# Kernel tuning notes

Measured on AMD Instinct MI355X. Metric: run time of the kernel, lower is better.

## Reference

```python
import jax, jax.numpy as jnp
import numpy as np

# Config constants (from init_kwargs)
B, T, D = 4, 2048, 2048      # batch, seq, d_model
E, R, F = 8, 8, 1024         # n_experts, gate_proj_rank, d_ff per expert
GATE_THRESHOLD = 0.0
GATE_TEMPERATURE = 1.0
W_INIT = 0.02                # standard small init scale


def setup_inputs() -> dict:
    key = jax.random.key(0)
    ks = jax.random.split(key, 6)
    hidden_states = jax.random.normal(ks[0], (B, T, D), jnp.float32)
    W_A = jax.random.normal(ks[1], (E, R, D), jnp.float32) * W_INIT      # low-rank gate proj per expert
    gate_scale = jnp.ones((E,), jnp.float32)
    # bias centered near typical score magnitude so the threshold mask is partially active
    gate_bias = 2.5 + 0.1 * jax.random.uniform(ks[2], (E,), jnp.float32)
    w_gate = jax.random.normal(ks[3], (E, F, D), jnp.float32) * W_INIT
    w_up = jax.random.normal(ks[4], (E, F, D), jnp.float32) * W_INIT
    w_down = jax.random.normal(ks[5], (E, D, F), jnp.float32) * W_INIT
    return {"hidden_states": hidden_states, "W_A": W_A, "gate_scale": gate_scale,
            "gate_bias": gate_bias, "w_gate": w_gate, "w_up": w_up, "w_down": w_down}


def reference(hidden_states, W_A, gate_scale, gate_bias, w_gate, w_up, w_down):
    orig_shape = hidden_states.shape
    x = hidden_states.reshape(-1, orig_shape[-1])                 # [N, D]
    threshold = GATE_THRESHOLD / GATE_TEMPERATURE

    # Shared low-rank gate projection for all experts (F.linear with concatenated W_A)
    gate_hidden = jnp.einsum('nd,erd->ner', x, W_A)               # [N, E, R]
    # _gate_norm: L2 norm over rank dim, divided by temperature -> [N, E]
    scores = jnp.sqrt(jnp.sum(gate_hidden * gate_hidden, axis=-1)) / GATE_TEMPERATURE
    # per-expert scale / bias
    scores = scores * gate_scale[None, :] - gate_bias[None, :]    # [N, E]
    mask = scores >= threshold                                    # [N, E] bool

    # Masked SwiGLU FFN per expert, vectorized over E (same math as the expert loop)
    h = jax.nn.silu(jnp.einsum('nd,efd->nef', x, w_gate)) * jnp.einsum('nd,efd->nef', x, w_up)  # [N, E, F]
    gate_w = jnp.where(mask, jax.nn.sigmoid(scores), 0.0)         # [N, E] masked gating weight
    out = jnp.einsum('nef,edf,ne->nd', h, w_down, gate_w)         # accumulate expert outputs
    out = out.reshape(orig_shape)

    # Scattered gate scores: -inf where expert inactive (stack over experts at dim=-1)
    score_full = jnp.where(mask, scores, -jnp.inf).reshape(orig_shape[:-1] + (E,))  # [B, T, E]
    return out, score_full
```

## Files before the change

### kernel.cpp

```cpp
#include <hip/hip_runtime.h>
#include <hip/hip_bf16.h>
#include <math.h>

#define NTOK   8192
#define DMODEL 2048
#define NEXP   8
#define RGATE  8
#define DFF    1024

#define NEG_SENTINEL (-3.0e38f)

using f32x4  = __attribute__((ext_vector_type(4))) float;
using short8 = __attribute__((ext_vector_type(8))) short;

static __device__ __forceinline__ short f2bf(float f) {
  union { float f; unsigned u; } v; v.f = f;
  unsigned r = v.u + 0x7fffu + ((v.u >> 16) & 1u);
  return (short)(r >> 16);
}
static __device__ __forceinline__ float bf2f(short s) {
  union { unsigned u; float f; } v; v.u = ((unsigned)(unsigned short)s) << 16;
  return v.f;
}
static __device__ __forceinline__ short8 cvt8(const float4 a, const float4 b) {
  short8 o;
  o[0] = f2bf(a.x); o[1] = f2bf(a.y); o[2] = f2bf(a.z); o[3] = f2bf(a.w);
  o[4] = f2bf(b.x); o[5] = f2bf(b.y); o[6] = f2bf(b.z); o[7] = f2bf(b.w);
  return o;
}

#define GLOAD_LDS(gp, lp)                                                  \
  __builtin_amdgcn_global_load_lds(                                        \
      (const __attribute__((address_space(1))) void*)(gp),                 \
      (__attribute__((address_space(3))) void*)(lp), 16, 0, 0)

__global__ __launch_bounds__(256) void prep_zero(
    float4* __restrict__ out4, int4* __restrict__ ic4, int nIc4, int zero_out) {
  const int stride = gridDim.x * blockDim.x;
  const float4 z4 = make_float4(0.f, 0.f, 0.f, 0.f);
  for (int i = blockIdx.x * blockDim.x + threadIdx.x;
       i < NTOK * DMODEL / 4; i += stride) {
    if (zero_out) out4[i] = z4;
    if (i < nIc4) ic4[i] = make_int4(0, 0, 0, 0);
    if (!zero_out && i >= nIc4) break;
  }
}

__global__ __launch_bounds__(256) void cvt_kernel(
    const float* __restrict__ in, short* __restrict__ out, int n8) {
  const int stride = gridDim.x * blockDim.x;
  for (int i = blockIdx.x * blockDim.x + threadIdx.x; i < n8; i += stride) {
    const float4 a = ((const float4*)in)[(size_t)i * 2];
    const float4 b = ((const float4*)in)[(size_t)i * 2 + 1];
    ((short8*)out)[i] = cvt8(a, b);
  }
}

__global__ __launch_bounds__(256) void pack_gu(
    const float* __restrict__ wg, const float* __restrict__ wu,
    short* __restrict__ wgu) {
  const int stride = gridDim.x * blockDim.x;
  const int total = NEXP * 2048 * (DMODEL / 8);
  for (int i = blockIdx.x * blockDim.x + threadIdx.x; i < total; i += stride) {
    const int c = i & 255;
    const int r = (i >> 8) & 2047;
    const int e = i >> 19;
    const int sel = (r >> 4) & 1;
    const int f = ((r >> 5) << 4) + (r & 15);
    const float* src = (sel ? wu : wg) + ((size_t)(e * DFF + f)) * DMODEL + c * 8;
    const float4 a = *(const float4*)src;
    const float4 b = *(const float4*)(src + 4);
    ((short8*)wgu)[i] = cvt8(a, b);
  }
}

__global__ __launch_bounds__(256) void gate_v3(
    const float* __restrict__ x, const float* __restrict__ W_A,
    const float* __restrict__ gscale, const float* __restrict__ gbias,
    float* __restrict__ gw, float* __restrict__ score_out,
    int* __restrict__ idx, int* __restrict__ pos, int* __restrict__ cnt) {
  __shared__ float ghs[32][65];
  const int tok0 = blockIdx.x * 32;
  const int t = threadIdx.x;
  const int ks = t & 3;
  const int posn = t >> 2;
  const int tg = posn & 7;
  const int rg = posn >> 3;
  const float* xp = x + (size_t)(tok0 + tg * 4) * DMODEL;
  const float* wp = W_A + (size_t)(rg * 8) * DMODEL;

  float acc[4][8];
#pragma unroll
  for (int i = 0; i < 4; ++i)
#pragma unroll
    for (int r = 0; r < 8; ++r) acc[i][r] = 0.f;

  float4 xa_[4], wa_[8], xb_[4], wb_[8];
  auto loadj = [&](int j, float4* xv, float4* wv) {
    const int k = ks * 4 + j * 16;
#pragma unroll
    for (int i = 0; i < 4; ++i) xv[i] = *(const float4*)(xp + (size_t)i * DMODEL + k);
#pragma unroll
    for (int r = 0; r < 8; ++r) wv[r] = *(const float4*)(wp + (size_t)r * DMODEL + k);
  };
  auto fmaj = [&](const float4* xv, const float4* wv) {
#pragma unroll
    for (int i = 0; i < 4; ++i)
#pragma unroll
      for (int r = 0; r < 8; ++r) {
        acc[i][r] = fmaf(xv[i].x, wv[r].x, acc[i][r]);
        acc[i][r] = fmaf(xv[i].y, wv[r].y, acc[i][r]);
        acc[i][r] = fmaf(xv[i].z, wv[r].z, acc[i][r]);
        acc[i][r] = fmaf(xv[i].w, wv[r].w, acc[i][r]);
      }
  };

  loadj(0, xa_, wa_);
#pragma unroll 1
  for (int j = 0; j < 128; j += 2) {
    loadj(j + 1, xb_, wb_);
    fmaj(xa_, wa_);
    if (j + 2 < 128) loadj(j + 2, xa_, wa_);
    fmaj(xb_, wb_);
  }

#pragma unroll
  for (int i = 0; i < 4; ++i)
#pragma unroll
    for (int r = 0; r < 8; ++r) {
      float v = acc[i][r];
      v += __shfl_xor(v, 1);
      v += __shfl_xor(v, 2);
      acc[i][r] = v;
    }
  if (ks == 0) {
#pragma unroll
    for (int i = 0; i < 4; ++i)
#pragma unroll
      for (int r = 0; r < 8; ++r) ghs[tg * 4 + i][rg * 8 + r] = acc[i][r];
  }
  __syncthreads();

  {
    const int tk = t >> 3, e = t & 7;
    const int n = tok0 + tk;
    float ss = 0.f;
#pragma unroll
    for (int r = 0; r < RGATE; ++r) { const float v = ghs[tk][e * 8 + r]; ss += v * v; }
    const float score = sqrtf(ss) * gscale[e] - gbias[e];
    const bool m = (score >= 0.0f);
    const float sig = 1.0f / (1.0f + expf(-score));
    gw[(size_t)n * NEXP + e] = m ? sig : 0.0f;
    score_out[(size_t)n * NEXP + e] = m ? score : NEG_SENTINEL;
    int slot = -1;
    if (m) {
      slot = atomicAdd(&cnt[e], 1);
      idx[(size_t)e * NTOK + slot] = n;
    }
    pos[(size_t)e * NTOK + n] = slot;
  }
}

#define FFN1_STAGE(AS, BS, k0)                                                 \
  _Pragma("unroll") for (int i_ = 0; i_ < 4; ++i_) {                           \
    const int row_ = wid * 32 + i_ * 8;                                        \
    GLOAD_LDS(xb + (size_t)tokA[i_] * DMODEL + (k0) + lk,                      \
              (char*)(AS) + row_ * 128);                                       \
    GLOAD_LDS(Bb + (size_t)(row_ + lr) * DMODEL + (k0) + lk,                   \
              (char*)(BS) + row_ * 128);                                       \
  }

#define FFN1_COMPUTE(AS, BS)                                                   \
  _Pragma("unroll") for (int ks_ = 0; ks_ < 2; ++ks_) {                        \
    const int cswz_ = ((ks_ * 4 + (lane >> 4)) ^ (lane & 7)) << 4;             \
    short8 af_[8], bf_[4];                                                     \
    _Pragma("unroll") for (int q_ = 0; q_ < 8; ++q_)                           \
      af_[q_] = *(const short8*)((const char*)(AS) +                           \
                (arow + q_ * 16 + (lane & 15)) * 128 + cswz_);                 \
    _Pragma("unroll") for (int q_ = 0; q_ < 4; ++q_)                           \
      bf_[q_] = *(const short8*)((const char*)(BS) +                           \
                (brow + q_ * 16 + (lane & 15)) * 128 + cswz_);                 \
    _Pragma("unroll") for (int nf_ = 0; nf_ < 8; ++nf_)                        \
      _Pragma("unroll") for (int ff_ = 0; ff_ < 4; ++ff_)                      \
        acc[nf_][ff_] = __builtin_amdgcn_mfma_f32_16x16x32_bf16(               \
            af_[nf_], bf_[ff_], acc[nf_][ff_], 0, 0, 0);                       \
  }

__global__ __launch_bounds__(512, 2) void ffn1_gemm256(
    const short* __restrict__ xb, const short* __restrict__ wgu,
    const int* __restrict__ idx, const int* __restrict__ cnt,
    const float* __restrict__ gw, short* __restrict__ Hb, int e_arg) {
  const int e = (e_arg < 0) ? (int)blockIdx.z : e_arg;
  short* __restrict__ Hbe = Hb + ((e_arg < 0) ? (size_t)e * NTOK * DFF : (size_t)0);
  const int cnte = cnt[e];
  const int n0 = blockIdx.y * 256;
  if (n0 >= cnte) return;

  __shared__ __align__(16) short As0[256 * 64];
  __shared__ __align__(16) short Bs0[256 * 64];
  __shared__ __align__(16) short As1[256 * 64];
  __shared__ __align__(16) short Bs1[256 * 64];

  const int c0 = blockIdx.x * 256;
  const int t = threadIdx.x, lane = t & 63, wid = t >> 6;
  const int arow = (wid >> 2) * 128;
  const int brow = (wid & 3) * 64;
  const int* idxe = idx + (size_t)e * NTOK;
  const short* Bb = wgu + (size_t)e * 2048 * DMODEL + (size_t)c0 * DMODEL;
  const int lr = lane >> 3;
  const int lk = ((lane & 7) ^ lr) * 8;

  int tokA[4];
#pragma unroll
  for (int i = 0; i < 4; ++i) tokA[i] = idxe[n0 + wid * 32 + i * 8 + lr];

  f32x4 acc[8][4];
#pragma unroll
  for (int i = 0; i < 8; ++i)
#pragma unroll
    for (int j = 0; j < 4; ++j) acc[i][j] = (f32x4){0.f, 0.f, 0.f, 0.f};

  FFN1_STAGE(As0, Bs0, 0);
  __syncthreads();
#pragma unroll 1
  for (int kt = 0; kt < 32; kt += 2) {
    FFN1_STAGE(As1, Bs1, (kt + 1) * 64);
    FFN1_COMPUTE(As0, Bs0);
    __syncthreads();
    if (kt + 2 < 32) FFN1_STAGE(As0, Bs0, (kt + 2) * 64);
    FFN1_COMPUTE(As1, Bs1);
    __syncthreads();
  }

  const int fhalf = c0 >> 1;
#pragma unroll
  for (int nf = 0; nf < 8; ++nf) {
#pragma unroll
    for (int j = 0; j < 4; ++j) {
      const int n = n0 + arow + nf * 16 + (lane >> 4) * 4 + j;
      const bool valid = n < cnte;
      const int tok = valid ? idxe[n] : 0;
      const float gwv = gw[(size_t)tok * NEXP + e];
#pragma unroll
      for (int p = 0; p < 2; ++p) {
        const float gv = acc[nf][2 * p][j];
        const float uv = acc[nf][2 * p + 1][j];
        const float h = (gv / (1.f + expf(-gv))) * uv * gwv;
        const int f = fhalf + ((wid & 3) * 2 + p) * 16 + (lane & 15);
        Hbe[(size_t)n * DFF + f] = valid ? f2bf(h) : (short)0;
      }
    }
  }
}

#define FFN2_STAGE(AS, BS, k0)                                                 \
  _Pragma("unroll") for (int i_ = 0; i_ < 4; ++i_) {                           \
    const int row_ = wid * 32 + i_ * 8;                                        \
    GLOAD_LDS(Ab + (size_t)(row_ + lr) * DFF + (k0) + lk,                      \
              (char*)(AS) + row_ * 128);                                       \
    GLOAD_LDS(Bb + (size_t)(row_ + lr) * DFF + (k0) + lk,                      \
              (char*)(BS) + row_ * 128);                                       \
  }

#define FFN2_COMPUTE(AS, BS)                                                   \
  _Pragma("unroll") for (int ks_ = 0; ks_ < 2; ++ks_) {                        \
    const int cswz_ = ((ks_ * 4 + (lane >> 4)) ^ (lane & 7)) << 4;             \
    short8 af_[4], bf_[4];                                                     \
    _Pragma("unroll") for (int q_ = 0; q_ < 4; ++q_) {                         \
      af_[q_] = *(const short8*)((const char*)(AS) +                           \
                (wr * 64 + q_ * 16 + (lane & 15)) * 128 + cswz_);              \
      bf_[q_] = *(const short8*)((const char*)(BS) +                           \
                (wc * 64 + q_ * 16 + (lane & 15)) * 128 + cswz_);              \
    }                                                                          \
    _Pragma("unroll") for (int nf_ = 0; nf_ < 4; ++nf_)                        \
      _Pragma("unroll") for (int ff_ = 0; ff_ < 4; ++ff_)                      \
        acc[nf_][ff_] = __builtin_amdgcn_mfma_f32_16x16x32_bf16(               \
            af_[nf_], bf_[ff_], acc[nf_][ff_], 0, 0, 0);                       \
  }

__global__ __launch_bounds__(256, 2) void ffn2z_gemm(
    const short* __restrict__ Hb, const short* __restrict__ wdb,
    const int* __restrict__ cnt, short* __restrict__ Cp, int e0) {
  const int e = e0 + blockIdx.z;
  const int cnte = cnt[e];
  const int n0 = blockIdx.y * 128;
  if (n0 >= cnte) return;
  __shared__ __align__(16) short As0[128 * 64];
  __shared__ __align__(16) short Bs0[128 * 64];
  __shared__ __align__(16) short As1[128 * 64];
  __shared__ __align__(16) short Bs1[128 * 64];

  const int c0 = blockIdx.x * 128;
  const int t = threadIdx.x, lane = t & 63, wid = t >> 6;
  const int wr = wid >> 1, wc = wid & 1;
  const short* Ab = Hb + (size_t)e * NTOK * DFF + (size_t)n0 * DFF;
  const short* Bb = wdb + (size_t)e * DMODEL * DFF + (size_t)c0 * DFF;
  short* Cpe = Cp + (size_t)blockIdx.z * NTOK * DMODEL;
  const int lr = lane >> 3;
  const int lk = ((lane & 7) ^ lr) * 8;

  f32x4 acc[4][4];
#pragma unroll
  for (int i = 0; i < 4; ++i)
#pragma unroll
    for (int j = 0; j < 4; ++j) acc[i][j] = (f32x4){0.f, 0.f, 0.f, 0.f};

  FFN2_STAGE(As0, Bs0, 0);
  __syncthreads();
#pragma unroll 1
  for (int kt = 0; kt < 16; kt += 2) {
    FFN2_STAGE(As1, Bs1, (kt + 1) * 64);
    FFN2_COMPUTE(As0, Bs0);
    __syncthreads();
    if (kt + 2 < 16) FFN2_STAGE(As0, Bs0, (kt + 2) * 64);
    FFN2_COMPUTE(As1, Bs1);
    __syncthreads();
  }

#pragma unroll
  for (int nf = 0; nf < 4; ++nf) {
#pragma unroll
    for (int j = 0; j < 4; ++j) {
      const int n = n0 + wr * 64 + nf * 16 + (lane >> 4) * 4 + j;
      if (n < cnte) {
#pragma unroll
        for (int ff = 0; ff < 4; ++ff) {
          const int d = c0 + wc * 64 + ff * 16 + (lane & 15);
          Cpe[(size_t)n * DMODEL + d] = f2bf(acc[nf][ff][j]);
        }
      }
    }
  }
}

__global__ __launch_bounds__(256) void reduce_out_g(
    const short* __restrict__ Cp, const int* __restrict__ pos,
    float* __restrict__ out, int e0, int ge, int accum) {
  const int n = blockIdx.x;
  const int t = threadIdx.x;
  float* op = out + (size_t)n * DMODEL + t * 8;
  float acc[8];
  if (accum) {
    const float4 a = *(const float4*)op;
    const float4 b = *(const float4*)(op + 4);
    acc[0] = a.x; acc[1] = a.y; acc[2] = a.z; acc[3] = a.w;
    acc[4] = b.x; acc[5] = b.y; acc[6] = b.z; acc[7] = b.w;
  } else {
#pragma unroll
    for (int j = 0; j < 8; ++j) acc[j] = 0.f;
  }
  for (int el = 0; el < ge; ++el) {
    const int p = pos[(size_t)(e0 + el) * NTOK + n];
    if (p >= 0) {
      const short8 v = *(const short8*)(Cp + (size_t)el * NTOK * DMODEL +
                                        (size_t)p * DMODEL + t * 8);
#pragma unroll
      for (int j = 0; j < 8; ++j) acc[j] += bf2f(v[j]);
    }
  }
  *(float4*)op = make_float4(acc[0], acc[1], acc[2], acc[3]);
  *(float4*)(op + 4) = make_float4(acc[4], acc[5], acc[6], acc[7]);
}

__global__ __launch_bounds__(256, 2) void ffn2_gemm_db(
    const short* __restrict__ Hbe, const short* __restrict__ wdb,
    const int* __restrict__ idx, const int* __restrict__ cnt,
    float* __restrict__ out, float* __restrict__ dummy, int e) {
  const int cnte = cnt[e];
  const int n0 = blockIdx.y * 128;
  if (n0 >= cnte) return;
  __shared__ __align__(16) short As0[128 * 64];
  __shared__ __align__(16) short Bs0[128 * 64];
  __shared__ __align__(16) short As1[128 * 64];
  __shared__ __align__(16) short Bs1[128 * 64];

  const int c0 = blockIdx.x * 128;
  const int t = threadIdx.x, lane = t & 63, wid = t >> 6;
  const int wr = wid >> 1, wc = wid & 1;
  const int* idxe = idx + (size_t)e * NTOK;
  const short* Ab = Hbe + (size_t)n0 * DFF;
  const short* Bb = wdb + (size_t)e * DMODEL * DFF + (size_t)c0 * DFF;
  const int lr = lane >> 3;
  const int lk = ((lane & 7) ^ lr) * 8;

  f32x4 acc[4][4];
#pragma unroll
  for (int i = 0; i < 4; ++i)
#pragma unroll
    for (int j = 0; j < 4; ++j) acc[i][j] = (f32x4){0.f, 0.f, 0.f, 0.f};

  FFN2_STAGE(As0, Bs0, 0);
  __syncthreads();
#pragma unroll 1
  for (int kt = 0; kt < 16; kt += 2) {
    FFN2_STAGE(As1, Bs1, (kt + 1) * 64);
    FFN2_COMPUTE(As0, Bs0);
    __syncthreads();
    if (kt + 2 < 16) FFN2_STAGE(As0, Bs0, (kt + 2) * 64);
    FFN2_COMPUTE(As1, Bs1);
    __syncthreads();
  }

#pragma unroll
  for (int nf = 0; nf < 4; ++nf) {
#pragma unroll
    for (int j = 0; j < 4; ++j) {
      const int n = n0 + wr * 64 + nf * 16 + (lane >> 4) * 4 + j;
      const bool valid = n < cnte;
      const int tok = valid ? idxe[n] : 0;
      float* bp = valid ? (out + (size_t)tok * DMODEL) : dummy;
#pragma unroll
      for (int ff = 0; ff < 4; ++ff) {
        const int d = c0 + wc * 64 + ff * 16 + (lane & 15);
        bp[valid ? d : (d & 2047)] += acc[nf][ff][j];
      }
    }
  }
}

extern "C" void kernel_launch(void* const* d_in, const int* in_sizes, int n_in,
                              void* d_out, int out_size, void* d_ws, size_t ws_size,
                              hipStream_t stream) {
  const float* x      = (const float*)d_in[0];
  const float* W_A    = (const float*)d_in[1];
  const float* gscale = (const float*)d_in[2];
  const float* gbias  = (const float*)d_in[3];
  const float* wg     = (const float*)d_in[4];
  const float* wu     = (const float*)d_in[5];
  const float* wd     = (const float*)d_in[6];

  float* out       = (float*)d_out;
  float* score_out = out + (size_t)NTOK * DMODEL;

  const size_t CNT = (size_t)16777216;
  const size_t CP_SLICE = (size_t)NTOK * DMODEL * 2;
  size_t off = 0;
  float* gw    = (float*)((char*)d_ws + off); off += (size_t)NTOK * NEXP * 4;
  int*   idx   = (int*)((char*)d_ws + off);   off += (size_t)NEXP * NTOK * 4;
  int*   pos   = (int*)((char*)d_ws + off);   off += (size_t)NEXP * NTOK * 4;
  int*   cnt   = (int*)((char*)d_ws + off);   off += 16 * 4;
  float* dummy = (float*)((char*)d_ws + off); off += (size_t)DMODEL * 4;
  short* wdb   = (short*)((char*)d_ws + off); off += CNT * 2;
  const size_t hb_off = off;
  short* Hb    = (short*)((char*)d_ws + off); off += (size_t)NEXP * NTOK * DFF * 2;
  const size_t xb_off = off;
  short* xb    = (short*)((char*)d_ws + off); off += CNT * 2;
  short* wgu   = (short*)((char*)d_ws + off); off += CNT * 4;
  const size_t needA = off;
  short* Cp    = (short*)((char*)d_ws + xb_off);

  const bool tierA = (ws_size >= needA);
  int G = 0;
  if (tierA) {
    size_t avail = ws_size - xb_off;
    G = (int)(avail / CP_SLICE);
    if (G > NEXP) G = NEXP;
  }

  short* HbB  = Hb;
  short* xbB  = (short*)((char*)d_ws + hb_off + (size_t)NTOK * DFF * 2);
  short* wguB = xbB + CNT;

  const int nIc4 = (int)((2 * NEXP * NTOK + 16) / 4);
  const int zero_out = (tierA && G >= 1) ? 0 : 1;
  prep_zero<<<2048, 256, 0, stream>>>((float4*)out, (int4*)idx, nIc4, zero_out);

  short* xbT  = tierA ? xb : xbB;
  short* wguT = tierA ? wgu : wguB;
  cvt_kernel<<<2048, 256, 0, stream>>>(x,  xbT,  (int)(CNT / 8));
  cvt_kernel<<<2048, 256, 0, stream>>>(wd, wdb, (int)(CNT / 8));
  pack_gu<<<2048, 256, 0, stream>>>(wg, wu, wguT);
  gate_v3<<<NTOK / 32, 256, 0, stream>>>(x, W_A, gscale, gbias, gw,
                                         score_out, idx, pos, cnt);

  if (tierA && G >= 1) {
    ffn1_gemm256<<<dim3(2048 / 256, NTOK / 256, NEXP), 512, 0, stream>>>(
        xb, wgu, idx, cnt, gw, Hb, -1);
    const int np = (NEXP + G - 1) / G;
    int e0 = 0;
    for (int p = 0; p < np; ++p) {
      const int rem_p = np - p;
      const int ge = (NEXP - e0 + rem_p - 1) / rem_p;
      ffn2z_gemm<<<dim3(DMODEL / 128, NTOK / 128, ge), 256, 0, stream>>>(
          Hb, wdb, cnt, Cp, e0);
      reduce_out_g<<<NTOK, 256, 0, stream>>>(Cp, pos, out, e0, ge, p > 0);
      e0 += ge;
    }
  } else if (tierA) {
    ffn1_gemm256<<<dim3(2048 / 256, NTOK / 256, NEXP), 512, 0, stream>>>(
        xb, wgu, idx, cnt, gw, Hb, -1);
    for (int e = 0; e < NEXP; ++e)
      ffn2_gemm_db<<<dim3(DMODEL / 128, NTOK / 128), 256, 0, stream>>>(
          Hb + (size_t)e * NTOK * DFF, wdb, idx, cnt, out, dummy, e);
  } else {
    for (int e = 0; e < NEXP; ++e) {
      ffn1_gemm256<<<dim3(2048 / 256, NTOK / 256), 512, 0, stream>>>(
          xbB, wguB, idx, cnt, gw, HbB, e);
      ffn2_gemm_db<<<dim3(DMODEL / 128, NTOK / 128), 256, 0, stream>>>(
          HbB, wdb, idx, cnt, out, dummy, e);
    }
  }
}
```

Baseline: 876.9 us.

## Fuse prep kernels into one and restructure MFMA loops with setprio

Merges the zeroing, x/w_down conversion and gate/up packing kernels into a single prep_all launch. It also stops clearing the idx buffer, resetting only the expert counters and clamping out-of-range token indices in ffn1. Both GEMM compute macros now load fragments for both k-steps up front, issue MFMAs in sub-blocks, and raise wave priority around the MFMA bursts. This cuts launch count and prep memory traffic, but the changed fragment ordering may raise register pressure in the GEMMs.

```diff
diff --git a/kernel.cpp b/kernel.cpp
--- a/kernel.cpp
+++ b/kernel.cpp
@@ -34,43 +34,42 @@
       (const __attribute__((address_space(1))) void*)(gp),                 \
       (__attribute__((address_space(3))) void*)(lp), 16, 0, 0)
 
-__global__ __launch_bounds__(256) void prep_zero(
-    float4* __restrict__ out4, int4* __restrict__ ic4, int nIc4, int zero_out) {
+#define SEG_CVT  2097152
+#define SEG_PACK 4194304
+__global__ __launch_bounds__(256) void prep_all(
+    const float* __restrict__ x, const float* __restrict__ wd,
+    const float* __restrict__ wg, const float* __restrict__ wu,
+    short* __restrict__ xb, short* __restrict__ wdb, short* __restrict__ wgu,
+    int* __restrict__ cnt, float4* __restrict__ out4, int zero_out) {
+  if (blockIdx.x == 0 && threadIdx.x < 16) cnt[threadIdx.x] = 0;
   const int stride = gridDim.x * blockDim.x;
-  const float4 z4 = make_float4(0.f, 0.f, 0.f, 0.f);
-  for (int i = blockIdx.x * blockDim.x + threadIdx.x;
-       i < NTOK * DMODEL / 4; i += stride) {
-    if (zero_out) out4[i] = z4;
-    if (i < nIc4) ic4[i] = make_int4(0, 0, 0, 0);
-    if (!zero_out && i >= nIc4) break;
-  }
-}
-
-__global__ __launch_bounds__(256) void cvt_kernel(
-    const float* __restrict__ in, short* __restrict__ out, int n8) {
-  const int stride = gridDim.x * blockDim.x;
-  for (int i = blockIdx.x * blockDim.x + threadIdx.x; i < n8; i += stride) {
-    const float4 a = ((const float4*)in)[(size_t)i * 2];
-    const float4 b = ((const float4*)in)[(size_t)i * 2 + 1];
-    ((short8*)out)[i] = cvt8(a, b);
-  }
-}
-
-__global__ __launch_bounds__(256) void pack_gu(
-    const float* __restrict__ wg, const float* __restrict__ wu,
-    short* __restrict__ wgu) {
-  const int stride = gridDim.x * blockDim.x;
-  const int total = NEXP * 2048 * (DMODEL / 8);
+  const int total = SEG_CVT * 2 + SEG_PACK + (zero_out ? SEG_CVT : 0);
   for (int i = blockIdx.x * blockDim.x + threadIdx.x; i < total; i += stride) {
-    const int c = i & 255;
-    const int r = (i >> 8) & 2047;
-    const int e = i >> 19;
-    const int sel = (r >> 4) & 1;
-    const int f = ((r >> 5) << 4) + (r & 15);
-    const float* src = (sel ? wu : wg) + ((size_t)(e * DFF + f)) * DMODEL + c * 8;
-    const float4 a = *(const float4*)src;
-    const float4 b = *(const float4*)(src + 4);
-    ((short8*)wgu)[i] = cvt8(a, b);
+    if (i < SEG_CVT) {
+      const float4 a = ((const float4*)x)[(size_t)i * 2];
+      const float4 b = ((const float4*)x)[(size_t)i * 2 + 1];
+      ((short8*)xb)[i] = cvt8(a, b);
+    } else if (i < 2 * SEG_CVT) {
+      const int j = i - SEG_CVT;
+      const float4 a = ((const float4*)wd)[(size_t)j * 2];
+      const float4 b = ((const float4*)wd)[(size_t)j * 2 + 1];
+      ((short8*)wdb)[j] = cvt8(a, b);
+    } else if (i < 2 * SEG_CVT + SEG_PACK) {
+      const int j = i - 2 * SEG_CVT;
+      const int c = j & 255;
+      const int r = (j >> 8) & 2047;
+      const int e = j >> 19;
+      const int sel = (r >> 4) & 1;
+      const int f = ((r >> 5) << 4) + (r & 15);
+      const float* src = (sel ? wu : wg) + ((size_t)(e * DFF + f)) * DMODEL + c * 8;
+      const float4 a = *(const float4*)src;
+      const float4 b = *(const float4*)(src + 4);
+      ((short8*)wgu)[j] = cvt8(a, b);
+    } else {
+      const int j = i - (2 * SEG_CVT + SEG_PACK);
+      out4[(size_t)j * 2] = make_float4(0.f, 0.f, 0.f, 0.f);
+      out4[(size_t)j * 2 + 1] = make_float4(0.f, 0.f, 0.f, 0.f);
+    }
   }
 }
 
@@ -170,20 +169,31 @@
               (char*)(BS) + row_ * 128);                                       \
   }
 
+#define CSWZ(ks_) ((((ks_) * 4 + (lane >> 4)) ^ (lane & 7)) << 4)
+
 #define FFN1_COMPUTE(AS, BS)                                                   \
-  _Pragma("unroll") for (int ks_ = 0; ks_ < 2; ++ks_) {                        \
-    const int cswz_ = ((ks_ * 4 + (lane >> 4)) ^ (lane & 7)) << 4;             \
-    short8 af_[8], bf_[4];                                                     \
-    _Pragma("unroll") for (int q_ = 0; q_ < 8; ++q_)                           \
-      af_[q_] = *(const short8*)((const char*)(AS) +                           \
-                (arow + q_ * 16 + (lane & 15)) * 128 + cswz_);                 \
+  _Pragma("unroll") for (int ah_ = 0; ah_ < 2; ++ah_) {                        \
+    short8 af_[4][2];                                                          \
     _Pragma("unroll") for (int q_ = 0; q_ < 4; ++q_)                           \
-      bf_[q_] = *(const short8*)((const char*)(BS) +                           \
-                (brow + q_ * 16 + (lane & 15)) * 128 + cswz_);                 \
-    _Pragma("unroll") for (int nf_ = 0; nf_ < 8; ++nf_)                        \
-      _Pragma("unroll") for (int ff_ = 0; ff_ < 4; ++ff_)                      \
-        acc[nf_][ff_] = __builtin_amdgcn_mfma_f32_16x16x32_bf16(               \
-            af_[nf_], bf_[ff_], acc[nf_][ff_], 0, 0, 0);                       \
+      _Pragma("unroll") for (int ks_ = 0; ks_ < 2; ++ks_)                      \
+        af_[q_][ks_] = *(const short8*)((const char*)(AS) +                    \
+            (arow + (ah_ * 4 + q_) * 16 + (lane & 15)) * 128 + CSWZ(ks_));     \
+    _Pragma("unroll") for (int bh_ = 0; bh_ < 2; ++bh_) {                      \
+      short8 bf_[2][2];                                                        \
+      _Pragma("unroll") for (int q_ = 0; q_ < 2; ++q_)                         \
+        _Pragma("unroll") for (int ks_ = 0; ks_ < 2; ++ks_)                    \
+          bf_[q_][ks_] = *(const short8*)((const char*)(BS) +                  \
+              (brow + (bh_ * 2 + q_) * 16 + (lane & 15)) * 128 + CSWZ(ks_));   \
+      __builtin_amdgcn_s_setprio(1);                                           \
+      _Pragma("unroll") for (int ks_ = 0; ks_ < 2; ++ks_)                      \
+        _Pragma("unroll") for (int nf_ = 0; nf_ < 4; ++nf_)                    \
+          _Pragma("unroll") for (int ff_ = 0; ff_ < 2; ++ff_)                  \
+            acc[ah_ * 4 + nf_][bh_ * 2 + ff_] =                                \
+                __builtin_amdgcn_mfma_f32_16x16x32_bf16(                       \
+                    af_[nf_][ks_], bf_[ff_][ks_],                              \
+                    acc[ah_ * 4 + nf_][bh_ * 2 + ff_], 0, 0, 0);               \
+      __builtin_amdgcn_s_setprio(0);                                           \
+    }                                                                          \
   }
 
 __global__ __launch_bounds__(512, 2) void ffn1_gemm256(
@@ -212,7 +222,11 @@
 
   int tokA[4];
 #pragma unroll
-  for (int i = 0; i < 4; ++i) tokA[i] = idxe[n0 + wid * 32 + i * 8 + lr];
+  for (int i = 0; i < 4; ++i) {
+    int n = n0 + wid * 32 + i * 8 + lr;
+    if (n >= cnte) n = cnte - 1;
+    tokA[i] = idxe[n];
+  }
 
   f32x4 acc[8][4];
 #pragma unroll
@@ -263,19 +277,28 @@
   }
 
 #define FFN2_COMPUTE(AS, BS)                                                   \
-  _Pragma("unroll") for (int ks_ = 0; ks_ < 2; ++ks_) {                        \
-    const int cswz_ = ((ks_ * 4 + (lane >> 4)) ^ (lane & 7)) << 4;             \
-    short8 af_[4], bf_[4];                                                     \
-    _Pragma("unroll") for (int q_ = 0; q_ < 4; ++q_) {                         \
-      af_[q_] = *(const short8*)((const char*)(AS) +                           \
-                (wr * 64 + q_ * 16 + (lane & 15)) * 128 + cswz_);              \
-      bf_[q_] = *(const short8*)((const char*)(BS) +                           \
-                (wc * 64 + q_ * 16 + (lane & 15)) * 128 + cswz_);              \
+  {                                                                            \
+    short8 af_[4][2];                                                          \
+    _Pragma("unroll") for (int q_ = 0; q_ < 4; ++q_)                           \
+      _Pragma("unroll") for (int ks_ = 0; ks_ < 2; ++ks_)                      \
+        af_[q_][ks_] = *(const short8*)((const char*)(AS) +                    \
+            (wr * 64 + q_ * 16 + (lane & 15)) * 128 + CSWZ(ks_));              \
+    _Pragma("unroll") for (int bh_ = 0; bh_ < 2; ++bh_) {                      \
+      short8 bf_[2][2];                                                        \
+      _Pragma("unroll") for (int q_ = 0; q_ < 2; ++q_)                         \
+        _Pragma("unroll") for (int ks_ = 0; ks_ < 2; ++ks_)                    \
+          bf_[q_][ks_] = *(const short8*)((const char*)(BS) +                  \
+              (wc * 64 + (bh_ * 2 + q_) * 16 + (lane & 15)) * 128 + CSWZ(ks_));\
+      __builtin_amdgcn_s_setprio(1);                                           \
+      _Pragma("unroll") for (int ks_ = 0; ks_ < 2; ++ks_)                      \
+        _Pragma("unroll") for (int nf_ = 0; nf_ < 4; ++nf_)                    \
+          _Pragma("unroll") for (int ff_ = 0; ff_ < 2; ++ff_)                  \
+            acc[nf_][bh_ * 2 + ff_] =                                          \
+                __builtin_amdgcn_mfma_f32_16x16x32_bf16(                       \
+                    af_[nf_][ks_], bf_[ff_][ks_],                              \
+                    acc[nf_][bh_ * 2 + ff_], 0, 0, 0);                         \
+      __builtin_amdgcn_s_setprio(0);                                           \
     }                                                                          \
-    _Pragma("unroll") for (int nf_ = 0; nf_ < 4; ++nf_)                        \
-      _Pragma("unroll") for (int ff_ = 0; ff_ < 4; ++ff_)                      \
-        acc[nf_][ff_] = __builtin_amdgcn_mfma_f32_16x16x32_bf16(               \
-            af_[nf_], bf_[ff_], acc[nf_][ff_], 0, 0, 0);                       \
   }
 
 __global__ __launch_bounds__(256, 2) void ffn2z_gemm(
@@ -461,15 +484,12 @@
   short* xbB  = (short*)((char*)d_ws + hb_off + (size_t)NTOK * DFF * 2);
   short* wguB = xbB + CNT;
 
-  const int nIc4 = (int)((2 * NEXP * NTOK + 16) / 4);
   const int zero_out = (tierA && G >= 1) ? 0 : 1;
-  prep_zero<<<2048, 256, 0, stream>>>((float4*)out, (int4*)idx, nIc4, zero_out);
-
   short* xbT  = tierA ? xb : xbB;
   short* wguT = tierA ? wgu : wguB;
-  cvt_kernel<<<2048, 256, 0, stream>>>(x,  xbT,  (int)(CNT / 8));
-  cvt_kernel<<<2048, 256, 0, stream>>>(wd, wdb, (int)(CNT / 8));
-  pack_gu<<<2048, 256, 0, stream>>>(wg, wu, wguT);
+
+  prep_all<<<2048, 256, 0, stream>>>(x, wd, wg, wu, xbT, wdb, wguT, cnt,
+                                     (float4*)out, zero_out);
   gate_v3<<<NTOK / 32, 256, 0, stream>>>(x, W_A, gscale, gbias, gw,
                                          score_out, idx, pos, cnt);
 
```

New measurement: 826.7 us. 5.7% less time.
